# Optimization experiments

Measured on AMD Instinct MI355X. Metric: run time of the kernel, lower is better.

The kernel has to match this reference:

```python
import jax, jax.numpy as jnp
import numpy as np

B, T = 128, 2048
E, OUT, HID = 8, 32, 64          # num_experts, kan_out_features, gru_hidden_dim
GRID_SIZE, ORDER = 5, 3          # standard efficient-kan defaults
KCOEF = GRID_SIZE + ORDER        # B-spline basis functions per input feature


def make_grid():
    # extended knot grid on [-1, 1], length GRID_SIZE + 2*ORDER + 1
    h = 2.0 / GRID_SIZE
    return jnp.arange(-ORDER, GRID_SIZE + ORDER + 1, dtype=jnp.float32) * h - 1.0


def b_splines(x, grid):
    # x: [..., in_features] -> [..., in_features, KCOEF] via Cox-de Boor recursion
    x = x[..., None]
    b = ((x >= grid[:-1]) & (x < grid[1:])).astype(x.dtype)
    for k in range(1, ORDER + 1):
        left = (x - grid[:-(k + 1)]) / (grid[k:-1] - grid[:-(k + 1)])
        right = (grid[k + 1:] - x) / (grid[k + 1:] - grid[1:-k])
        b = left * b[..., :-1] + right * b[..., 1:]
    return b


def kan_moe(x, gate_w, gate_b, base_w, spline_w, grid):
    # x: [B,T,in=1]; dense softmax-gated mixture of KANLinear experts
    gate = jax.nn.softmax(x @ gate_w + gate_b, axis=-1)                 # [B,T,E]
    base_out = jnp.einsum('bti,eoi->bteo', jax.nn.silu(x), base_w)      # [B,T,E,OUT]
    bs = b_splines(x, grid).reshape(x.shape[0], x.shape[1], -1)         # [B,T,in*KCOEF]
    spline_out = jnp.einsum('btk,eok->bteo', bs, spline_w)              # [B,T,E,OUT]
    return jnp.einsum('bte,bteo->bto', gate, base_out + spline_out)     # [B,T,OUT]


def gru(x, w_ih, w_hh, b_ih, b_hh):
    # PyTorch GRU convention: gates ordered (r, z, n); batch_first semantics
    xp = jnp.einsum('btf,gf->btg', x, w_ih) + b_ih                      # [B,T,3H]

    def step(h, xt):
        hp = h @ w_hh.T + b_hh
        xr, xz, xn = jnp.split(xt, 3, axis=-1)
        hr, hz, hn = jnp.split(hp, 3, axis=-1)
        r = jax.nn.sigmoid(xr + hr)
        z = jax.nn.sigmoid(xz + hz)
        n = jnp.tanh(xn + r * hn)
        h = (1.0 - z) * n + z * h
        return h, h

    h0 = jnp.zeros((x.shape[0], HID), x.dtype)
    _, hs = jax.lax.scan(step, h0, jnp.swapaxes(xp, 0, 1))
    return jnp.swapaxes(hs, 0, 1)                                       # [B,T,H]


def setup_inputs() -> dict:
    key = jax.random.key(0)
    ks = jax.random.split(key, 12)
    def n(k, shape, scale=0.1):
        return jax.random.normal(k, shape, jnp.float32) * scale
    return {
        'a': jax.random.normal(ks[0], (B, T, 1), jnp.float32),
        'd': jax.random.normal(ks[1], (B, T, 1), jnp.float32),
        'gate_w_a': n(ks[2], (1, E)), 'gate_b_a': jnp.zeros((E,), jnp.float32),
        'base_w_a': n(ks[3], (E, OUT, 1)), 'spline_w_a': n(ks[4], (E, OUT, KCOEF)),
        'gate_w_d': n(ks[5], (1, E)), 'gate_b_d': jnp.zeros((E,), jnp.float32),
        'base_w_d': n(ks[6], (E, OUT, 1)), 'spline_w_d': n(ks[7], (E, OUT, KCOEF)),
        'conv_w': n(ks[8], (OUT, OUT, 5)), 'conv_b': jnp.zeros((OUT,), jnp.float32),
        'w_ih': n(ks[9], (3 * HID, OUT)), 'w_hh': n(ks[10], (3 * HID, HID)),
        'b_ih': jnp.zeros((3 * HID,), jnp.float32), 'b_hh': jnp.zeros((3 * HID,), jnp.float32),
    }


def reference(a, d, gate_w_a, gate_b_a, base_w_a, spline_w_a,
              gate_w_d, gate_b_d, base_w_d, spline_w_d,
              conv_w, conv_b, w_ih, w_hh, b_ih, b_hh):
    grid = make_grid()
    fa = kan_moe(a, gate_w_a, gate_b_a, base_w_a, spline_w_a, grid)     # trend features
    fd = kan_moe(d, gate_w_d, gate_b_d, base_w_d, spline_w_d, grid)     # residual features
    # TemporalBlock: permute -> Conv1d(padding='same') -> ReLU -> permute back
    xc = jnp.swapaxes(fa, 1, 2)                                         # [B,C,T]
    yc = jax.lax.conv_general_dilated(
        xc, conv_w, (1,), 'SAME', dimension_numbers=('NCH', 'OIH', 'NCH')
    ) + conv_b[None, :, None]
    trend = jnp.swapaxes(jax.nn.relu(yc), 1, 2)                         # [B,T,OUT]
    ctx = gru(fd, w_ih, w_hh, b_ih, b_hh)                               # [B,T,HID]
    # dropout is identity in eval mode
    return jnp.concatenate([trend, ctx], axis=-1)                       # [B,T,OUT+HID]
```

## Files before the change

### kernel.cpp

```cpp
#include <hip/hip_runtime.h>
#include <cstdint>

typedef _Float16 half2_t __attribute__((ext_vector_type(2)));

#define B_   128
#define T_   2048
#define E_   8
#define OUT_ 32
#define HID_ 64
#define KC_  8
#define TILE_A 128
#define NSEG 4
#define SEGT (T_ / NSEG)
#define WUPC 4
#define CH_  32

__device__ __forceinline__ float frcp(float x) { return __builtin_amdgcn_rcpf(x); }
__device__ __forceinline__ float exp2_(float x) {
#if __has_builtin(__builtin_amdgcn_exp2f)
  return __builtin_amdgcn_exp2f(x);
#else
  return exp2f(x);
#endif
}
__device__ __forceinline__ float fsig(float x) { return frcp(1.0f + __expf(-x)); }

__device__ __forceinline__ float fdot2_(half2_t a, half2_t b, float c) {
#if __has_builtin(__builtin_amdgcn_fdot2)
  return __builtin_amdgcn_fdot2(a, b, c, false);
#else
  return fmaf((float)a.x, (float)b.x, fmaf((float)a.y, (float)b.y, c));
#endif
}

__device__ __forceinline__ half2_t u2h2(unsigned u) {
  return __builtin_bit_cast(half2_t, u);
}
__device__ __forceinline__ half2_t packh2(float a, float b) {
  half2_t h; h.x = (_Float16)a; h.y = (_Float16)b; return h;
}

#define NLOG2E  (-1.4426950408889634f)
#define N2LOG2E (-2.8853900817779268f)

__device__ __forceinline__ void kan_scalars(float x, const float* gwr, const float* gbr,
                                            float& silu, float* gate, float* bs) {
  silu = x * fsig(x);
  float le[E_];
  float m = -1e30f;
#pragma unroll
  for (int e = 0; e < E_; ++e) { le[e] = fmaf(x, gwr[e], gbr[e]); m = fmaxf(m, le[e]); }
  float s = 0.f;
#pragma unroll
  for (int e = 0; e < E_; ++e) { gate[e] = __expf(le[e] - m); s += gate[e]; }
  float inv = frcp(s);
#pragma unroll
  for (int e = 0; e < E_; ++e) gate[e] *= inv;
  float g[12];
#pragma unroll
  for (int i = 0; i < 12; ++i) g[i] = (float)(i - 3) * 0.4f - 1.0f;
  float bb[11];
#pragma unroll
  for (int i = 0; i < 11; ++i) bb[i] = (x >= g[i] && x < g[i + 1]) ? 1.0f : 0.0f;
#pragma unroll
  for (int k = 1; k <= 3; ++k) {
#pragma unroll
    for (int i = 0; i < 11 - k; ++i) {
      const float dl = 1.0f / (g[i + k] - g[i]);
      const float dr = 1.0f / (g[i + k + 1] - g[i + 1]);
      float left  = (x - g[i]) * dl;
      float right = (g[i + k + 1] - x) * dr;
      bb[i] = left * bb[i] + right * bb[i + 1];
    }
  }
#pragma unroll
  for (int i = 0; i < KC_; ++i) bs[i] = bb[i];
}

__global__ __launch_bounds__(256, 1) void fused3_kernel(
    const float* __restrict__ a, const float* __restrict__ d,
    const float* __restrict__ gwa, const float* __restrict__ gba,
    const float* __restrict__ bwa, const float* __restrict__ swa,
    const float* __restrict__ gwd, const float* __restrict__ gbd,
    const float* __restrict__ bwd, const float* __restrict__ swd,
    const float* __restrict__ cw, const float* __restrict__ cb,
    const float* __restrict__ wih_g, const float* __restrict__ whh_g,
    const float* __restrict__ bih_g, const float* __restrict__ bhh_g,
    float* __restrict__ out)
{
  __shared__ __align__(16) char smem_[47360];
  const int tid = threadIdx.x;

  if (blockIdx.x < NSEG * B_) {
    auto xqrz   = (unsigned (*)[CH_][64])smem_;
    auto xqn    = (_Float16 (*)[CH_][64])(smem_ + 16384);
    auto packsw = (float (*)[CH_][16])(smem_ + 24576);
    auto hbc    = (unsigned short*)(smem_ + 30720);

    const int b = blockIdx.x & (B_ - 1);
    const int seg = blockIdx.x >> 7;
    const int tstart = (seg == 0) ? 0 : (seg * SEGT - WUPC * CH_);
    const int wup = (seg == 0) ? 0 : WUPC;
    const int nch = ((seg == 0) ? SEGT : (SEGT + WUPC * CH_)) / CH_;
    const int w = tid >> 6;
    const int ln = tid & 63;
    const size_t db = (size_t)b * T_;
    float* outrow = out + db * 96 + 32;
    const uint4* hq4 = (const uint4*)hbc;

    half2_t whhp[3][32];
    float bhh3[3];
    uint4 u0, u1, u2, u3, u4, u5, u6, u7;
    if (w == 0) {
#pragma unroll
      for (int g3 = 0; g3 < 3; ++g3) {
        const float sc = (g3 == 2) ? N2LOG2E : NLOG2E;
        const int g = g3 * 64 + ln;
#pragma unroll
        for (int i = 0; i < 64; i += 4) {
          const float4 v = *(const float4*)&whh_g[(size_t)g * 64 + i];
          whhp[g3][i / 2]     = packh2(v.x * sc, v.y * sc);
          whhp[g3][i / 2 + 1] = packh2(v.z * sc, v.w * sc);
        }
        bhh3[g3] = bhh_g[g] * sc;
      }
      hbc[ln] = __builtin_bit_cast(unsigned short, (_Float16)0.0f);
      asm volatile("" ::: "memory");
      u0 = hq4[0]; u1 = hq4[1]; u2 = hq4[2]; u3 = hq4[3];
      u4 = hq4[4]; u5 = hq4[5]; u6 = hq4[6]; u7 = hq4[7];
    }

    float A_[E_];
    half2_t Beh[E_][4];
    float bihr = 0.f;
    float gwrd[E_], gbrd[E_];
    const int p3 = (w >= 1) ? (w - 1) : 0;
    if (w >= 1) {
      const float sc = (p3 == 2) ? N2LOG2E : NLOG2E;
      const int g = p3 * 64 + ln;
      float wihr[32];
#pragma unroll
      for (int i = 0; i < 32; i += 4) {
        float4 v = *(const float4*)&wih_g[(size_t)g * 32 + i];
        wihr[i] = v.x * sc; wihr[i + 1] = v.y * sc;
        wihr[i + 2] = v.z * sc; wihr[i + 3] = v.w * sc;
      }
      bihr = bih_g[g] * sc;
#pragma unroll
      for (int e = 0; e < E_; ++e) { gwrd[e] = gwd[e]; gbrd[e] = gbd[e]; }
#pragma unroll
      for (int e = 0; e < E_; ++e) {
        float acc = 0.f;
#pragma unroll 4
        for (int c = 0; c < 32; c += 4) {
          const float4 bv = *(const float4*)&bwd[e * OUT_ + c];
          acc = fmaf(wihr[c], bv.x, acc);
          acc = fmaf(wihr[c + 1], bv.y, acc);
          acc = fmaf(wihr[c + 2], bv.z, acc);
          acc = fmaf(wihr[c + 3], bv.w, acc);
        }
        A_[e] = acc;
      }
#pragma unroll
      for (int e = 0; e < E_; ++e) {
        float bk[KC_];
#pragma unroll
        for (int k = 0; k < KC_; ++k) bk[k] = 0.f;
#pragma unroll 4
        for (int c = 0; c < 32; ++c) {
          const float4 s0 = *(const float4*)&swd[(e * OUT_ + c) * KC_ + 0];
          const float4 s1 = *(const float4*)&swd[(e * OUT_ + c) * KC_ + 4];
          const float wc = wihr[c];
          bk[0] = fmaf(wc, s0.x, bk[0]); bk[1] = fmaf(wc, s0.y, bk[1]);
          bk[2] = fmaf(wc, s0.z, bk[2]); bk[3] = fmaf(wc, s0.w, bk[3]);
          bk[4] = fmaf(wc, s1.x, bk[4]); bk[5] = fmaf(wc, s1.y, bk[5]);
          bk[6] = fmaf(wc, s1.z, bk[6]); bk[7] = fmaf(wc, s1.w, bk[7]);
        }
#pragma unroll
        for (int q = 0; q < 4; ++q) Beh[e][q] = packh2(bk[2 * q], bk[2 * q + 1]);
      }
    }

    float h = 0.0f;

    for (int ic = 0; ic <= nch; ++ic) {
      if (w >= 1 && ic < nch) {
        const int p = ic & 1;
        if (ln < CH_) {
          const float x = d[db + tstart + ic * CH_ + ln];
          float silu, gate[E_], bs[KC_];
          kan_scalars(x, gwrd, gbrd, silu, gate, bs);
          float* prow = &packsw[p3][ln][0];
          *(float4*)&prow[0] = *(float4*)&gate[0];
          *(float4*)&prow[4] = *(float4*)&gate[4];
          prow[8] = silu;
          half2_t* bsp = (half2_t*)&prow[10];
#pragma unroll
          for (int q = 0; q < 4; ++q) bsp[q] = packh2(bs[2 * q], bs[2 * q + 1]);
        }
        asm volatile("" ::: "memory");
#pragma unroll 2
        for (int t = 0; t < CH_; ++t) {
          const float* pr = &packsw[p3][t][0];
          const float4 g0 = *(const float4*)&pr[0];
          const float4 g1 = *(const float4*)&pr[4];
          const float silu_t = pr[8];
          const half2_t* bsp = (const half2_t*)&pr[10];
          const half2_t b0 = bsp[0], b1 = bsp[1], b2 = bsp[2], b3 = bsp[3];
          float acc = bihr;
          {
            float in0 = silu_t * A_[0];
            in0 = fdot2_(b0, Beh[0][0], in0); in0 = fdot2_(b1, Beh[0][1], in0);
            in0 = fdot2_(b2, Beh[0][2], in0); in0 = fdot2_(b3, Beh[0][3], in0);
            acc = fmaf(g0.x, in0, acc);
            float in1 = silu_t * A_[1];
            in1 = fdot2_(b0, Beh[1][0], in1); in1 = fdot2_(b1, Beh[1][1], in1);
            in1 = fdot2_(b2, Beh[1][2], in1); in1 = fdot2_(b3, Beh[1][3], in1);
            acc = fmaf(g0.y, in1, acc);
            float in2 = silu_t * A_[2];
            in2 = fdot2_(b0, Beh[2][0], in2); in2 = fdot2_(b1, Beh[2][1], in2);
            in2 = fdot2_(b2, Beh[2][2], in2); in2 = fdot2_(b3, Beh[2][3], in2);
            acc = fmaf(g0.z, in2, acc);
            float in3 = silu_t * A_[3];
            in3 = fdot2_(b0, Beh[3][0], in3); in3 = fdot2_(b1, Beh[3][1], in3);
            in3 = fdot2_(b2, Beh[3][2], in3); in3 = fdot2_(b3, Beh[3][3], in3);
            acc = fmaf(g0.w, in3, acc);
            float in4 = silu_t * A_[4];
            in4 = fdot2_(b0, Beh[4][0], in4); in4 = fdot2_(b1, Beh[4][1], in4);
            in4 = fdot2_(b2, Beh[4][2], in4); in4 = fdot2_(b3, Beh[4][3], in4);
            acc = fmaf(g1.x, in4, acc);
            float in5 = silu_t * A_[5];
            in5 = fdot2_(b0, Beh[5][0], in5); in5 = fdot2_(b1, Beh[5][1], in5);
            in5 = fdot2_(b2, Beh[5][2], in5); in5 = fdot2_(b3, Beh[5][3], in5);
            acc = fmaf(g1.y, in5, acc);
            float in6 = silu_t * A_[6];
            in6 = fdot2_(b0, Beh[6][0], in6); in6 = fdot2_(b1, Beh[6][1], in6);
            in6 = fdot2_(b2, Beh[6][2], in6); in6 = fdot2_(b3, Beh[6][3], in6);
            acc = fmaf(g1.z, in6, acc);
            float in7 = silu_t * A_[7];
            in7 = fdot2_(b0, Beh[7][0], in7); in7 = fdot2_(b1, Beh[7][1], in7);
            in7 = fdot2_(b2, Beh[7][2], in7); in7 = fdot2_(b3, Beh[7][3], in7);
            acc = fmaf(g1.w, in7, acc);
          }
          if (p3 == 0)      ((_Float16*)&xqrz[p][t][ln])[0] = (_Float16)acc;
          else if (p3 == 1) ((_Float16*)&xqrz[p][t][ln])[1] = (_Float16)acc;
          else              xqn[p][t][ln] = (_Float16)acc;
        }
      }

      if (w == 0 && ic >= 1) {
        const int jc = ic - 1;
        const int p = jc & 1;
        const int tb = tstart + jc * CH_;
        const bool do_store = (jc >= wup);
        half2_t rz0 = u2h2(xqrz[p][0][ln]);
        float xr = (float)rz0.x, xz = (float)rz0.y;
        float xn = (float)xqn[p][0][ln];
        __builtin_amdgcn_s_setprio(1);
#pragma unroll 1
        for (int s = 0; s < CH_; ++s) {
          float ar0 = bhh3[0], ar1 = xr, ar2 = 0.f, ar3 = 0.f;
          float az0 = bhh3[1], az1 = xz, az2 = 0.f, az3 = 0.f;
          float an0 = bhh3[2], an1 = 0.f, an2 = 0.f, an3 = 0.f;
          {
            const half2_t q0 = u2h2(u0.x), q1 = u2h2(u0.y), q2 = u2h2(u0.z), q3 = u2h2(u0.w);
            ar0 = fdot2_(whhp[0][0], q0, ar0); ar1 = fdot2_(whhp[0][1], q1, ar1);
            ar2 = fdot2_(whhp[0][2], q2, ar2); ar3 = fdot2_(whhp[0][3], q3, ar3);
            az0 = fdot2_(whhp[1][0], q0, az0); az1 = fdot2_(whhp[1][1], q1, az1);
            az2 = fdot2_(whhp[1][2], q2, az2); az3 = fdot2_(whhp[1][3], q3, az3);
            an0 = fdot2_(whhp[2][0], q0, an0); an1 = fdot2_(whhp[2][1], q1, an1);
            an2 = fdot2_(whhp[2][2], q2, an2); an3 = fdot2_(whhp[2][3], q3, an3);
          }
          {
            const half2_t q0 = u2h2(u1.x), q1 = u2h2(u1.y), q2 = u2h2(u1.z), q3 = u2h2(u1.w);
            ar0 = fdot2_(whhp[0][4], q0, ar0); ar1 = fdot2_(whhp[0][5], q1, ar1);
            ar2 = fdot2_(whhp[0][6], q2, ar2); ar3 = fdot2_(whhp[0][7], q3, ar3);
            az0 = fdot2_(whhp[1][4], q0, az0); az1 = fdot2_(whhp[1][5], q1, az1);
            az2 = fdot2_(whhp[1][6], q2, az2); az3 = fdot2_(whhp[1][7], q3, az3);
            an0 = fdot2_(whhp[2][4], q0, an0); an1 = fdot2_(whhp[2][5], q1, an1);
            an2 = fdot2_(whhp[2][6], q2, an2); an3 = fdot2_(whhp[2][7], q3, an3);
          }
          {
            const half2_t q0 = u2h2(u2.x), q1 = u2h2(u2.y), q2 = u2h2(u2.z), q3 = u2h2(u2.w);
            ar0 = fdot2_(whhp[0][8], q0, ar0); ar1 = fdot2_(whhp[0][9], q1, ar1);
            ar2 = fdot2_(whhp[0][10], q2, ar2); ar3 = fdot2_(whhp[0][11], q3, ar3);
            az0 = fdot2_(whhp[1][8], q0, az0); az1 = fdot2_(whhp[1][9], q1, az1);
            az2 = fdot2_(whhp[1][10], q2, az2); az3 = fdot2_(whhp[1][11], q3, az3);
            an0 = fdot2_(whhp[2][8], q0, an0); an1 = fdot2_(whhp[2][9], q1, an1);
            an2 = fdot2_(whhp[2][10], q2, an2); an3 = fdot2_(whhp[2][11], q3, an3);
          }
          {
            const half2_t q0 = u2h2(u3.x), q1 = u2h2(u3.y), q2 = u2h2(u3.z), q3 = u2h2(u3.w);
            ar0 = fdot2_(whhp[0][12], q0, ar0); ar1 = fdot2_(whhp[0][13], q1, ar1);
            ar2 = fdot2_(whhp[0][14], q2, ar2); ar3 = fdot2_(whhp[0][15], q3, ar3);
            az0 = fdot2_(whhp[1][12], q0, az0); az1 = fdot2_(whhp[1][13], q1, az1);
            az2 = fdot2_(whhp[1][14], q2, az2); az3 = fdot2_(whhp[1][15], q3, az3);
            an0 = fdot2_(whhp[2][12], q0, an0); an1 = fdot2_(whhp[2][13], q1, an1);
            an2 = fdot2_(whhp[2][14], q2, an2); an3 = fdot2_(whhp[2][15], q3, an3);
          }
          {
            const half2_t q0 = u2h2(u4.x), q1 = u2h2(u4.y), q2 = u2h2(u4.z), q3 = u2h2(u4.w);
            ar0 = fdot2_(whhp[0][16], q0, ar0); ar1 = fdot2_(whhp[0][17], q1, ar1);
            ar2 = fdot2_(whhp[0][18], q2, ar2); ar3 = fdot2_(whhp[0][19], q3, ar3);
            az0 = fdot2_(whhp[1][16], q0, az0); az1 = fdot2_(whhp[1][17], q1, az1);
            az2 = fdot2_(whhp[1][18], q2, az2); az3 = fdot2_(whhp[1][19], q3, az3);
            an0 = fdot2_(whhp[2][16], q0, an0); an1 = fdot2_(whhp[2][17], q1, an1);
            an2 = fdot2_(whhp[2][18], q2, an2); an3 = fdot2_(whhp[2][19], q3, an3);
          }
          {
            const half2_t q0 = u2h2(u5.x), q1 = u2h2(u5.y), q2 = u2h2(u5.z), q3 = u2h2(u5.w);
            ar0 = fdot2_(whhp[0][20], q0, ar0); ar1 = fdot2_(whhp[0][21], q1, ar1);
            ar2 = fdot2_(whhp[0][22], q2, ar2); ar3 = fdot2_(whhp[0][23], q3, ar3);
            az0 = fdot2_(whhp[1][20], q0, az0); az1 = fdot2_(whhp[1][21], q1, az1);
            az2 = fdot2_(whhp[1][22], q2, az2); az3 = fdot2_(whhp[1][23], q3, az3);
            an0 = fdot2_(whhp[2][20], q0, an0); an1 = fdot2_(whhp[2][21], q1, an1);
            an2 = fdot2_(whhp[2][22], q2, an2); an3 = fdot2_(whhp[2][23], q3, an3);
          }
          {
            const half2_t q0 = u2h2(u6.x), q1 = u2h2(u6.y), q2 = u2h2(u6.z), q3 = u2h2(u6.w);
            ar0 = fdot2_(whhp[0][24], q0, ar0); ar1 = fdot2_(whhp[0][25], q1, ar1);
            ar2 = fdot2_(whhp[0][26], q2, ar2); ar3 = fdot2_(whhp[0][27], q3, ar3);
            az0 = fdot2_(whhp[1][24], q0, az0); az1 = fdot2_(whhp[1][25], q1, az1);
            az2 = fdot2_(whhp[1][26], q2, az2); az3 = fdot2_(whhp[1][27], q3, az3);
            an0 = fdot2_(whhp[2][24], q0, an0); an1 = fdot2_(whhp[2][25], q1, an1);
            an2 = fdot2_(whhp[2][26], q2, an2); an3 = fdot2_(whhp[2][27], q3, an3);
          }
          {
            const half2_t q0 = u2h2(u7.x), q1 = u2h2(u7.y), q2 = u2h2(u7.z), q3 = u2h2(u7.w);
            ar0 = fdot2_(whhp[0][28], q0, ar0); ar1 = fdot2_(whhp[0][29], q1, ar1);
            ar2 = fdot2_(whhp[0][30], q2, ar2); ar3 = fdot2_(whhp[0][31], q3, ar3);
            az0 = fdot2_(whhp[1][28], q0, az0); az1 = fdot2_(whhp[1][29], q1, az1);
            az2 = fdot2_(whhp[1][30], q2, az2); az3 = fdot2_(whhp[1][31], q3, az3);
            an0 = fdot2_(whhp[2][28], q0, an0); an1 = fdot2_(whhp[2][29], q1, an1);
            an2 = fdot2_(whhp[2][30], q2, an2); an3 = fdot2_(whhp[2][31], q3, an3);
          }
          const float hr = (ar0 + ar1) + (ar2 + ar3);
          const float hz = (az0 + az1) + (az2 + az3);
          const float hn = (an0 + an1) + (an2 + an3);
          const float r = frcp(1.0f + exp2_(hr));
          const float z = frcp(1.0f + exp2_(hz));
          const float tn = frcp(1.0f + exp2_(fmaf(r, hn, xn)));
          const float n = fmaf(2.0f, tn, -1.0f);
          h = n + z * (h - n);
          hbc[ln] = __builtin_bit_cast(unsigned short, (_Float16)h);
          asm volatile("" ::: "memory");
          const int sn = (s + 1) & (CH_ - 1);
          const unsigned rzn = xqrz[p][sn][ln];
          const _Float16 xnn = xqn[p][sn][ln];
          u0 = hq4[0]; u1 = hq4[1]; u2 = hq4[2]; u3 = hq4[3];
          u4 = hq4[4]; u5 = hq4[5]; u6 = hq4[6]; u7 = hq4[7];
          asm volatile("" ::: "memory");
          if (do_store) outrow[(size_t)(tb + s) * 96 + ln] = h;
          const half2_t rzh = u2h2(rzn);
          xr = (float)rzh.x; xz = (float)rzh.y; xn = (float)xnn;
        }
        __builtin_amdgcn_s_setprio(0);
      }
      __syncthreads();
    }
  } else {
    auto fa  = (float (*)[136])smem_;
    auto cwl = (float (*)[161])(smem_ + 17408);
    auto swl = (float (*)[OUT_][KC_])(smem_ + 38016);
    auto bwl = (float (*)[OUT_])(smem_ + 46208);
    float* gwl = (float*)(smem_ + 47232);
    float* gbl = (float*)(smem_ + 47264);

    for (int i = tid; i < OUT_ * OUT_ * 5; i += 256) cwl[i / 160][i % 160] = cw[i];
    for (int i = tid; i < E_ * OUT_ * KC_; i += 256) ((float*)swl)[i] = swa[i];
    for (int i = tid; i < E_ * OUT_; i += 256) ((float*)bwl)[i] = bwa[i];
    if (tid < E_) { gwl[tid] = gwa[tid]; gbl[tid] = gba[tid]; }
    __syncthreads();

    const int cid = blockIdx.x - NSEG * B_;
#pragma unroll 1
    for (int it = 0; it < 16; ++it) {
      const int gt = cid + it * 128;
      const int bb = gt >> 4;
      const int t0 = (gt & 15) * TILE_A;
      if (tid < TILE_A + 4) {
        const int i = tid;
        const int t = t0 + i - 2;
        const bool inr = (t >= 0) && (t < T_);
        const float x = inr ? a[(size_t)bb * T_ + t] : 0.0f;
        float gwr[E_], gbr[E_];
#pragma unroll
        for (int e = 0; e < E_; ++e) { gwr[e] = gwl[e]; gbr[e] = gbl[e]; }
        float silu, gate[E_], bs[KC_];
        kan_scalars(x, gwr, gbr, silu, gate, bs);
#pragma unroll 4
        for (int cc = 0; cc < OUT_; ++cc) {
          float accb = 0.f, accs = 0.f;
#pragma unroll
          for (int e = 0; e < E_; ++e) {
            accb = fmaf(gate[e], bwl[e][cc], accb);
            const float4 s0 = *(const float4*)&swl[e][cc][0];
            const float4 s1 = *(const float4*)&swl[e][cc][4];
            float dot = bs[0]*s0.x + bs[1]*s0.y + bs[2]*s0.z + bs[3]*s0.w
                      + bs[4]*s1.x + bs[5]*s1.y + bs[6]*s1.z + bs[7]*s1.w;
            accs = fmaf(gate[e], dot, accs);
          }
          fa[cc][i] = inr ? fmaf(silu, accb, accs) : 0.0f;
        }
      }
      __syncthreads();
      {
        const int o = tid & 31;
        const int grp = tid >> 5;
        const float bias = cb[o];
        float acc[16];
#pragma unroll
        for (int q = 0; q < 16; ++q) acc[q] = bias;
        for (int c = 0; c < OUT_; ++c) {
          float col[20];
#pragma unroll
          for (int q = 0; q < 5; ++q)
            *(float4*)&col[q * 4] = *(const float4*)&fa[c][grp * 16 + q * 4];
#pragma unroll
          for (int jj = 0; jj < 5; ++jj) {
            const float wv = cwl[o][c * 5 + jj];
#pragma unroll
            for (int q = 0; q < 16; ++q) acc[q] = fmaf(col[q + jj], wv, acc[q]);
          }
        }
#pragma unroll
        for (int q = 0; q < 16; ++q) {
          const int t = t0 + grp * 16 + q;
          out[((size_t)bb * T_ + t) * 96 + o] = fmaxf(acc[q], 0.0f);
        }
      }
      __syncthreads();
    }
  }
}

extern "C" void kernel_launch(void* const* d_in, const int* in_sizes, int n_in,
                              void* d_out, int out_size, void* d_ws, size_t ws_size,
                              hipStream_t stream) {
  (void)in_sizes; (void)n_in; (void)out_size; (void)d_ws; (void)ws_size;
  const float* a        = (const float*)d_in[0];
  const float* d        = (const float*)d_in[1];
  const float* gate_w_a = (const float*)d_in[2];
  const float* gate_b_a = (const float*)d_in[3];
  const float* base_w_a = (const float*)d_in[4];
  const float* spln_w_a = (const float*)d_in[5];
  const float* gate_w_d = (const float*)d_in[6];
  const float* gate_b_d = (const float*)d_in[7];
  const float* base_w_d = (const float*)d_in[8];
  const float* spln_w_d = (const float*)d_in[9];
  const float* conv_w   = (const float*)d_in[10];
  const float* conv_b   = (const float*)d_in[11];
  const float* w_ih     = (const float*)d_in[12];
  const float* w_hh     = (const float*)d_in[13];
  const float* b_ih     = (const float*)d_in[14];
  const float* b_hh     = (const float*)d_in[15];
  float* out = (float*)d_out;

  fused3_kernel<<<NSEG * B_ + B_, 256, 0, stream>>>(
      a, d, gate_w_a, gate_b_a, base_w_a, spln_w_a,
      gate_w_d, gate_b_d, base_w_d, spln_w_d,
      conv_w, conv_b, w_ih, w_hh, b_ih, b_hh, out);
}
```

Measured before the change: 650.9 us.

## Halve GRU time segments and fold conv trend work into each GRU block

```diff
diff --git a/kernel.cpp b/kernel.cpp
--- a/kernel.cpp
+++ b/kernel.cpp
@@ -10,10 +10,11 @@
 #define HID_ 64
 #define KC_  8
 #define TILE_A 128
-#define NSEG 4
-#define SEGT (T_ / NSEG)
-#define WUPC 4
-#define CH_  32
+#define NSEG 2
+#define SPLIT 1088
+#define WUPC 2
+#define CH_  64
+#define NCHB 17
 
 __device__ __forceinline__ float frcp(float x) { return __builtin_amdgcn_rcpf(x); }
 __device__ __forceinline__ float exp2_(float x) {
@@ -77,7 +78,7 @@
   for (int i = 0; i < KC_; ++i) bs[i] = bb[i];
 }
 
-__global__ __launch_bounds__(256, 1) void fused3_kernel(
+__global__ __launch_bounds__(256, 1) void fused5_kernel(
     const float* __restrict__ a, const float* __restrict__ d,
     const float* __restrict__ gwa, const float* __restrict__ gba,
     const float* __restrict__ bwa, const float* __restrict__ swa,
@@ -88,277 +89,277 @@
     const float* __restrict__ bih_g, const float* __restrict__ bhh_g,
     float* __restrict__ out)
 {
-  __shared__ __align__(16) char smem_[47360];
+  __shared__ __align__(16) char smem_[61568];
   const int tid = threadIdx.x;
 
-  if (blockIdx.x < NSEG * B_) {
-    auto xqrz   = (unsigned (*)[CH_][64])smem_;
-    auto xqn    = (_Float16 (*)[CH_][64])(smem_ + 16384);
-    auto packsw = (float (*)[CH_][16])(smem_ + 24576);
-    auto hbc    = (unsigned short*)(smem_ + 30720);
-
-    const int b = blockIdx.x & (B_ - 1);
-    const int seg = blockIdx.x >> 7;
-    const int tstart = (seg == 0) ? 0 : (seg * SEGT - WUPC * CH_);
-    const int wup = (seg == 0) ? 0 : WUPC;
-    const int nch = ((seg == 0) ? SEGT : (SEGT + WUPC * CH_)) / CH_;
-    const int w = tid >> 6;
-    const int ln = tid & 63;
-    const size_t db = (size_t)b * T_;
-    float* outrow = out + db * 96 + 32;
-    const uint4* hq4 = (const uint4*)hbc;
-
-    half2_t whhp[3][32];
-    float bhh3[3];
-    uint4 u0, u1, u2, u3, u4, u5, u6, u7;
-    if (w == 0) {
-#pragma unroll
-      for (int g3 = 0; g3 < 3; ++g3) {
-        const float sc = (g3 == 2) ? N2LOG2E : NLOG2E;
-        const int g = g3 * 64 + ln;
-#pragma unroll
-        for (int i = 0; i < 64; i += 4) {
-          const float4 v = *(const float4*)&whh_g[(size_t)g * 64 + i];
-          whhp[g3][i / 2]     = packh2(v.x * sc, v.y * sc);
-          whhp[g3][i / 2 + 1] = packh2(v.z * sc, v.w * sc);
-        }
-        bhh3[g3] = bhh_g[g] * sc;
-      }
-      hbc[ln] = __builtin_bit_cast(unsigned short, (_Float16)0.0f);
+  auto xqrz   = (unsigned (*)[CH_][64])smem_;
+  auto xqn    = (_Float16 (*)[CH_][64])(smem_ + 32768);
+  auto packsw = (float (*)[CH_][16])(smem_ + 49152);
+  auto hbc    = (unsigned short*)(smem_ + 61440);
+
+  const int bid = (int)blockIdx.x;
+  const int b = bid & (B_ - 1);
+  const int seg = bid >> 7;
+  const int tstart = (seg == 0) ? 0 : (SPLIT - WUPC * CH_);
+  const int wup = (seg == 0) ? 0 : WUPC;
+  const int w = tid >> 6;
+  const int ln = tid & 63;
+  const size_t db = (size_t)b * T_;
+  float* outrow = out + db * 96 + 32;
+  const uint4* hq4 = (const uint4*)hbc;
+
+  half2_t whhp[3][32];
+  float bhh3[3];
+  uint4 u0, u1, u2, u3, u4, u5, u6, u7;
+  if (w == 0) {
+#pragma unroll
+    for (int g3 = 0; g3 < 3; ++g3) {
+      const float sc = (g3 == 2) ? N2LOG2E : NLOG2E;
+      const int g = g3 * 64 + ln;
+#pragma unroll
+      for (int i = 0; i < 64; i += 4) {
+        const float4 v = *(const float4*)&whh_g[(size_t)g * 64 + i];
+        whhp[g3][i / 2]     = packh2(v.x * sc, v.y * sc);
+        whhp[g3][i / 2 + 1] = packh2(v.z * sc, v.w * sc);
+      }
+      bhh3[g3] = bhh_g[g] * sc;
+    }
+    hbc[ln] = __builtin_bit_cast(unsigned short, (_Float16)0.0f);
+    asm volatile("" ::: "memory");
+    u0 = hq4[0]; u1 = hq4[1]; u2 = hq4[2]; u3 = hq4[3];
+    u4 = hq4[4]; u5 = hq4[5]; u6 = hq4[6]; u7 = hq4[7];
+  }
+
+  float A_[E_];
+  half2_t Beh[E_][4];
+  float bihr = 0.f;
+  float gwrd[E_], gbrd[E_];
+  const int p3 = (w >= 1) ? (w - 1) : 0;
+  if (w >= 1) {
+    const float sc = (p3 == 2) ? N2LOG2E : NLOG2E;
+    const int g = p3 * 64 + ln;
+    float wihr[32];
+#pragma unroll
+    for (int i = 0; i < 32; i += 4) {
+      float4 v = *(const float4*)&wih_g[(size_t)g * 32 + i];
+      wihr[i] = v.x * sc; wihr[i + 1] = v.y * sc;
+      wihr[i + 2] = v.z * sc; wihr[i + 3] = v.w * sc;
+    }
+    bihr = bih_g[g] * sc;
+#pragma unroll
+    for (int e = 0; e < E_; ++e) { gwrd[e] = gwd[e]; gbrd[e] = gbd[e]; }
+#pragma unroll
+    for (int e = 0; e < E_; ++e) {
+      float acc = 0.f;
+#pragma unroll 4
+      for (int c = 0; c < 32; c += 4) {
+        const float4 bv = *(const float4*)&bwd[e * OUT_ + c];
+        acc = fmaf(wihr[c], bv.x, acc);
+        acc = fmaf(wihr[c + 1], bv.y, acc);
+        acc = fmaf(wihr[c + 2], bv.z, acc);
+        acc = fmaf(wihr[c + 3], bv.w, acc);
+      }
+      A_[e] = acc;
+    }
+#pragma unroll
+    for (int e = 0; e < E_; ++e) {
+      float bk[KC_];
+#pragma unroll
+      for (int k = 0; k < KC_; ++k) bk[k] = 0.f;
+#pragma unroll 4
+      for (int c = 0; c < 32; ++c) {
+        const float4 s0 = *(const float4*)&swd[(e * OUT_ + c) * KC_ + 0];
+        const float4 s1 = *(const float4*)&swd[(e * OUT_ + c) * KC_ + 4];
+        const float wc = wihr[c];
+        bk[0] = fmaf(wc, s0.x, bk[0]); bk[1] = fmaf(wc, s0.y, bk[1]);
+        bk[2] = fmaf(wc, s0.z, bk[2]); bk[3] = fmaf(wc, s0.w, bk[3]);
+        bk[4] = fmaf(wc, s1.x, bk[4]); bk[5] = fmaf(wc, s1.y, bk[5]);
+        bk[6] = fmaf(wc, s1.z, bk[6]); bk[7] = fmaf(wc, s1.w, bk[7]);
+      }
+#pragma unroll
+      for (int q = 0; q < 4; ++q) Beh[e][q] = packh2(bk[2 * q], bk[2 * q + 1]);
+    }
+  }
+
+  float h = 0.0f;
+
+  for (int ic = 0; ic <= NCHB; ++ic) {
+    if (w >= 1 && ic < NCHB) {
+      const int p = ic & 1;
+      {
+        const float x = d[db + tstart + ic * CH_ + ln];
+        float silu, gate[E_], bs[KC_];
+        kan_scalars(x, gwrd, gbrd, silu, gate, bs);
+        float* prow = &packsw[p3][ln][0];
+        *(float4*)&prow[0] = *(float4*)&gate[0];
+        *(float4*)&prow[4] = *(float4*)&gate[4];
+        prow[8] = silu;
+        half2_t* bsp = (half2_t*)&prow[10];
+#pragma unroll
+        for (int q = 0; q < 4; ++q) bsp[q] = packh2(bs[2 * q], bs[2 * q + 1]);
+      }
       asm volatile("" ::: "memory");
-      u0 = hq4[0]; u1 = hq4[1]; u2 = hq4[2]; u3 = hq4[3];
-      u4 = hq4[4]; u5 = hq4[5]; u6 = hq4[6]; u7 = hq4[7];
-    }
-
-    float A_[E_];
-    half2_t Beh[E_][4];
-    float bihr = 0.f;
-    float gwrd[E_], gbrd[E_];
-    const int p3 = (w >= 1) ? (w - 1) : 0;
-    if (w >= 1) {
-      const float sc = (p3 == 2) ? N2LOG2E : NLOG2E;
-      const int g = p3 * 64 + ln;
-      float wihr[32];
-#pragma unroll
-      for (int i = 0; i < 32; i += 4) {
-        float4 v = *(const float4*)&wih_g[(size_t)g * 32 + i];
-        wihr[i] = v.x * sc; wihr[i + 1] = v.y * sc;
-        wihr[i + 2] = v.z * sc; wihr[i + 3] = v.w * sc;
-      }
-      bihr = bih_g[g] * sc;
-#pragma unroll
-      for (int e = 0; e < E_; ++e) { gwrd[e] = gwd[e]; gbrd[e] = gbd[e]; }
-#pragma unroll
-      for (int e = 0; e < E_; ++e) {
-        float acc = 0.f;
-#pragma unroll 4
-        for (int c = 0; c < 32; c += 4) {
-          const float4 bv = *(const float4*)&bwd[e * OUT_ + c];
-          acc = fmaf(wihr[c], bv.x, acc);
-          acc = fmaf(wihr[c + 1], bv.y, acc);
-          acc = fmaf(wihr[c + 2], bv.z, acc);
-          acc = fmaf(wihr[c + 3], bv.w, acc);
-        }
-        A_[e] = acc;
-      }
-#pragma unroll
-      for (int e = 0; e < E_; ++e) {
-        float bk[KC_];
-#pragma unroll
-        for (int k = 0; k < KC_; ++k) bk[k] = 0.f;
-#pragma unroll 4
-        for (int c = 0; c < 32; ++c) {
-          const float4 s0 = *(const float4*)&swd[(e * OUT_ + c) * KC_ + 0];
-          const float4 s1 = *(const float4*)&swd[(e * OUT_ + c) * KC_ + 4];
-          const float wc = wihr[c];
-          bk[0] = fmaf(wc, s0.x, bk[0]); bk[1] = fmaf(wc, s0.y, bk[1]);
-          bk[2] = fmaf(wc, s0.z, bk[2]); bk[3] = fmaf(wc, s0.w, bk[3]);
-          bk[4] = fmaf(wc, s1.x, bk[4]); bk[5] = fmaf(wc, s1.y, bk[5]);
-          bk[6] = fmaf(wc, s1.z, bk[6]); bk[7] = fmaf(wc, s1.w, bk[7]);
-        }
-#pragma unroll
-        for (int q = 0; q < 4; ++q) Beh[e][q] = packh2(bk[2 * q], bk[2 * q + 1]);
-      }
-    }
-
-    float h = 0.0f;
-
-    for (int ic = 0; ic <= nch; ++ic) {
-      if (w >= 1 && ic < nch) {
-        const int p = ic & 1;
-        if (ln < CH_) {
-          const float x = d[db + tstart + ic * CH_ + ln];
-          float silu, gate[E_], bs[KC_];
-          kan_scalars(x, gwrd, gbrd, silu, gate, bs);
-          float* prow = &packsw[p3][ln][0];
-          *(float4*)&prow[0] = *(float4*)&gate[0];
-          *(float4*)&prow[4] = *(float4*)&gate[4];
-          prow[8] = silu;
-          half2_t* bsp = (half2_t*)&prow[10];
-#pragma unroll
-          for (int q = 0; q < 4; ++q) bsp[q] = packh2(bs[2 * q], bs[2 * q + 1]);
-        }
+#pragma unroll 2
+      for (int t = 0; t < CH_; ++t) {
+        const float* pr = &packsw[p3][t][0];
+        const float4 g0 = *(const float4*)&pr[0];
+        const float4 g1 = *(const float4*)&pr[4];
+        const float silu_t = pr[8];
+        const half2_t* bsp = (const half2_t*)&pr[10];
+        const half2_t b0 = bsp[0], b1 = bsp[1], b2 = bsp[2], b3 = bsp[3];
+        float acc = bihr;
+        {
+          float in0 = silu_t * A_[0];
+          in0 = fdot2_(b0, Beh[0][0], in0); in0 = fdot2_(b1, Beh[0][1], in0);
+          in0 = fdot2_(b2, Beh[0][2], in0); in0 = fdot2_(b3, Beh[0][3], in0);
+          acc = fmaf(g0.x, in0, acc);
+          float in1 = silu_t * A_[1];
+          in1 = fdot2_(b0, Beh[1][0], in1); in1 = fdot2_(b1, Beh[1][1], in1);
+          in1 = fdot2_(b2, Beh[1][2], in1); in1 = fdot2_(b3, Beh[1][3], in1);
+          acc = fmaf(g0.y, in1, acc);
+          float in2 = silu_t * A_[2];
+          in2 = fdot2_(b0, Beh[2][0], in2); in2 = fdot2_(b1, Beh[2][1], in2);
+          in2 = fdot2_(b2, Beh[2][2], in2); in2 = fdot2_(b3, Beh[2][3], in2);
+          acc = fmaf(g0.z, in2, acc);
+          float in3 = silu_t * A_[3];
+          in3 = fdot2_(b0, Beh[3][0], in3); in3 = fdot2_(b1, Beh[3][1], in3);
+          in3 = fdot2_(b2, Beh[3][2], in3); in3 = fdot2_(b3, Beh[3][3], in3);
+          acc = fmaf(g0.w, in3, acc);
+          float in4 = silu_t * A_[4];
+          in4 = fdot2_(b0, Beh[4][0], in4); in4 = fdot2_(b1, Beh[4][1], in4);
+          in4 = fdot2_(b2, Beh[4][2], in4); in4 = fdot2_(b3, Beh[4][3], in4);
+          acc = fmaf(g1.x, in4, acc);
+          float in5 = silu_t * A_[5];
+          in5 = fdot2_(b0, Beh[5][0], in5); in5 = fdot2_(b1, Beh[5][1], in5);
+          in5 = fdot2_(b2, Beh[5][2], in5); in5 = fdot2_(b3, Beh[5][3], in5);
+          acc = fmaf(g1.y, in5, acc);
+          float in6 = silu_t * A_[6];
+          in6 = fdot2_(b0, Beh[6][0], in6); in6 = fdot2_(b1, Beh[6][1], in6);
+          in6 = fdot2_(b2, Beh[6][2], in6); in6 = fdot2_(b3, Beh[6][3], in6);
+          acc = fmaf(g1.z, in6, acc);
+          float in7 = silu_t * A_[7];
+          in7 = fdot2_(b0, Beh[7][0], in7); in7 = fdot2_(b1, Beh[7][1], in7);
+          in7 = fdot2_(b2, Beh[7][2], in7); in7 = fdot2_(b3, Beh[7][3], in7);
+          acc = fmaf(g1.w, in7, acc);
+        }
+        if (p3 == 0)      ((_Float16*)&xqrz[p][t][ln])[0] = (_Float16)acc;
+        else if (p3 == 1) ((_Float16*)&xqrz[p][t][ln])[1] = (_Float16)acc;
+        else              xqn[p][t][ln] = (_Float16)acc;
+      }
+    }
+
+    if (w == 0 && ic >= 1) {
+      const int jc = ic - 1;
+      const int p = jc & 1;
+      const int tb = tstart + jc * CH_;
+      const bool do_store = (jc >= wup);
+      half2_t rz0 = u2h2(xqrz[p][0][ln]);
+      float xr = (float)rz0.x, xz = (float)rz0.y;
+      float xn = (float)xqn[p][0][ln];
+      __builtin_amdgcn_s_setprio(1);
+#pragma unroll 1
+      for (int s = 0; s < CH_; ++s) {
+        float ar0 = bhh3[0], ar1 = xr, ar2 = 0.f, ar3 = 0.f;
+        float az0 = bhh3[1], az1 = xz, az2 = 0.f, az3 = 0.f;
+        float an0 = bhh3[2], an1 = 0.f, an2 = 0.f, an3 = 0.f;
+        {
+          const half2_t q0 = u2h2(u0.x), q1 = u2h2(u0.y), q2 = u2h2(u0.z), q3 = u2h2(u0.w);
+          ar0 = fdot2_(whhp[0][0], q0, ar0); ar1 = fdot2_(whhp[0][1], q1, ar1);
+          ar2 = fdot2_(whhp[0][2], q2, ar2); ar3 = fdot2_(whhp[0][3], q3, ar3);
+          az0 = fdot2_(whhp[1][0], q0, az0); az1 = fdot2_(whhp[1][1], q1, az1);
+          az2 = fdot2_(whhp[1][2], q2, az2); az3 = fdot2_(whhp[1][3], q3, az3);
+          an0 = fdot2_(whhp[2][0], q0, an0); an1 = fdot2_(whhp[2][1], q1, an1);
+          an2 = fdot2_(whhp[2][2], q2, an2); an3 = fdot2_(whhp[2][3], q3, an3);
+        }
+        {
+          const half2_t q0 = u2h2(u1.x), q1 = u2h2(u1.y), q2 = u2h2(u1.z), q3 = u2h2(u1.w);
+          ar0 = fdot2_(whhp[0][4], q0, ar0); ar1 = fdot2_(whhp[0][5], q1, ar1);
+          ar2 = fdot2_(whhp[0][6], q2, ar2); ar3 = fdot2_(whhp[0][7], q3, ar3);
+          az0 = fdot2_(whhp[1][4], q0, az0); az1 = fdot2_(whhp[1][5], q1, az1);
+          az2 = fdot2_(whhp[1][6], q2, az2); az3 = fdot2_(whhp[1][7], q3, az3);
+          an0 = fdot2_(whhp[2][4], q0, an0); an1 = fdot2_(whhp[2][5], q1, an1);
+          an2 = fdot2_(whhp[2][6], q2, an2); an3 = fdot2_(whhp[2][7], q3, an3);
+        }
+        {
+          const half2_t q0 = u2h2(u2.x), q1 = u2h2(u2.y), q2 = u2h2(u2.z), q3 = u2h2(u2.w);
+          ar0 = fdot2_(whhp[0][8], q0, ar0); ar1 = fdot2_(whhp[0][9], q1, ar1);
+          ar2 = fdot2_(whhp[0][10], q2, ar2); ar3 = fdot2_(whhp[0][11], q3, ar3);
+          az0 = fdot2_(whhp[1][8], q0, az0); az1 = fdot2_(whhp[1][9], q1, az1);
+          az2 = fdot2_(whhp[1][10], q2, az2); az3 = fdot2_(whhp[1][11], q3, az3);
+          an0 = fdot2_(whhp[2][8], q0, an0); an1 = fdot2_(whhp[2][9], q1, an1);
+          an2 = fdot2_(whhp[2][10], q2, an2); an3 = fdot2_(whhp[2][11], q3, an3);
+        }
+        {
+          const half2_t q0 = u2h2(u3.x), q1 = u2h2(u3.y), q2 = u2h2(u3.z), q3 = u2h2(u3.w);
+          ar0 = fdot2_(whhp[0][12], q0, ar0); ar1 = fdot2_(whhp[0][13], q1, ar1);
+          ar2 = fdot2_(whhp[0][14], q2, ar2); ar3 = fdot2_(whhp[0][15], q3, ar3);
+          az0 = fdot2_(whhp[1][12], q0, az0); az1 = fdot2_(whhp[1][13], q1, az1);
+          az2 = fdot2_(whhp[1][14], q2, az2); az3 = fdot2_(whhp[1][15], q3, az3);
+          an0 = fdot2_(whhp[2][12], q0, an0); an1 = fdot2_(whhp[2][13], q1, an1);
+          an2 = fdot2_(whhp[2][14], q2, an2); an3 = fdot2_(whhp[2][15], q3, an3);
+        }
+        {
+          const half2_t q0 = u2h2(u4.x), q1 = u2h2(u4.y), q2 = u2h2(u4.z), q3 = u2h2(u4.w);
+          ar0 = fdot2_(whhp[0][16], q0, ar0); ar1 = fdot2_(whhp[0][17], q1, ar1);
+          ar2 = fdot2_(whhp[0][18], q2, ar2); ar3 = fdot2_(whhp[0][19], q3, ar3);
+          az0 = fdot2_(whhp[1][16], q0, az0); az1 = fdot2_(whhp[1][17], q1, az1);
+          az2 = fdot2_(whhp[1][18], q2, az2); az3 = fdot2_(whhp[1][19], q3, az3);
+          an0 = fdot2_(whhp[2][16], q0, an0); an1 = fdot2_(whhp[2][17], q1, an1);
+          an2 = fdot2_(whhp[2][18], q2, an2); an3 = fdot2_(whhp[2][19], q3, an3);
+        }
+        {
+          const half2_t q0 = u2h2(u5.x), q1 = u2h2(u5.y), q2 = u2h2(u5.z), q3 = u2h2(u5.w);
+          ar0 = fdot2_(whhp[0][20], q0, ar0); ar1 = fdot2_(whhp[0][21], q1, ar1);
+          ar2 = fdot2_(whhp[0][22], q2, ar2); ar3 = fdot2_(whhp[0][23], q3, ar3);
+          az0 = fdot2_(whhp[1][20], q0, az0); az1 = fdot2_(whhp[1][21], q1, az1);
+          az2 = fdot2_(whhp[1][22], q2, az2); az3 = fdot2_(whhp[1][23], q3, az3);
+          an0 = fdot2_(whhp[2][20], q0, an0); an1 = fdot2_(whhp[2][21], q1, an1);
+          an2 = fdot2_(whhp[2][22], q2, an2); an3 = fdot2_(whhp[2][23], q3, an3);
+        }
+        {
+          const half2_t q0 = u2h2(u6.x), q1 = u2h2(u6.y), q2 = u2h2(u6.z), q3 = u2h2(u6.w);
+          ar0 = fdot2_(whhp[0][24], q0, ar0); ar1 = fdot2_(whhp[0][25], q1, ar1);
+          ar2 = fdot2_(whhp[0][26], q2, ar2); ar3 = fdot2_(whhp[0][27], q3, ar3);
+          az0 = fdot2_(whhp[1][24], q0, az0); az1 = fdot2_(whhp[1][25], q1, az1);
+          az2 = fdot2_(whhp[1][26], q2, az2); az3 = fdot2_(whhp[1][27], q3, az3);
+          an0 = fdot2_(whhp[2][24], q0, an0); an1 = fdot2_(whhp[2][25], q1, an1);
+          an2 = fdot2_(whhp[2][26], q2, an2); an3 = fdot2_(whhp[2][27], q3, an3);
+        }
+        {
+          const half2_t q0 = u2h2(u7.x), q1 = u2h2(u7.y), q2 = u2h2(u7.z), q3 = u2h2(u7.w);
+          ar0 = fdot2_(whhp[0][28], q0, ar0); ar1 = fdot2_(whhp[0][29], q1, ar1);
+          ar2 = fdot2_(whhp[0][30], q2, ar2); ar3 = fdot2_(whhp[0][31], q3, ar3);
+          az0 = fdot2_(whhp[1][28], q0, az0); az1 = fdot2_(whhp[1][29], q1, az1);
+          az2 = fdot2_(whhp[1][30], q2, az2); az3 = fdot2_(whhp[1][31], q3, az3);
+          an0 = fdot2_(whhp[2][28], q0, an0); an1 = fdot2_(whhp[2][29], q1, an1);
+          an2 = fdot2_(whhp[2][30], q2, an2); an3 = fdot2_(whhp[2][31], q3, an3);
+        }
+        const float hr = (ar0 + ar1) + (ar2 + ar3);
+        const float hz = (az0 + az1) + (az2 + az3);
+        const float hn = (an0 + an1) + (an2 + an3);
+        const float r = frcp(1.0f + exp2_(hr));
+        const float z = frcp(1.0f + exp2_(hz));
+        const float tn = frcp(1.0f + exp2_(fmaf(r, hn, xn)));
+        const float n = fmaf(2.0f, tn, -1.0f);
+        h = n + z * (h - n);
+        hbc[ln] = __builtin_bit_cast(unsigned short, (_Float16)h);
         asm volatile("" ::: "memory");
-#pragma unroll 2
-        for (int t = 0; t < CH_; ++t) {
-          const float* pr = &packsw[p3][t][0];
-          const float4 g0 = *(const float4*)&pr[0];
-          const float4 g1 = *(const float4*)&pr[4];
-          const float silu_t = pr[8];
-          const half2_t* bsp = (const half2_t*)&pr[10];
-          const half2_t b0 = bsp[0], b1 = bsp[1], b2 = bsp[2], b3 = bsp[3];
-          float acc = bihr;
-          {
-            float in0 = silu_t * A_[0];
-            in0 = fdot2_(b0, Beh[0][0], in0); in0 = fdot2_(b1, Beh[0][1], in0);
-            in0 = fdot2_(b2, Beh[0][2], in0); in0 = fdot2_(b3, Beh[0][3], in0);
-            acc = fmaf(g0.x, in0, acc);
-            float in1 = silu_t * A_[1];
-            in1 = fdot2_(b0, Beh[1][0], in1); in1 = fdot2_(b1, Beh[1][1], in1);
-            in1 = fdot2_(b2, Beh[1][2], in1); in1 = fdot2_(b3, Beh[1][3], in1);
-            acc = fmaf(g0.y, in1, acc);
-            float in2 = silu_t * A_[2];
-            in2 = fdot2_(b0, Beh[2][0], in2); in2 = fdot2_(b1, Beh[2][1], in2);
-            in2 = fdot2_(b2, Beh[2][2], in2); in2 = fdot2_(b3, Beh[2][3], in2);
-            acc = fmaf(g0.z, in2, acc);
-            float in3 = silu_t * A_[3];
-            in3 = fdot2_(b0, Beh[3][0], in3); in3 = fdot2_(b1, Beh[3][1], in3);
-            in3 = fdot2_(b2, Beh[3][2], in3); in3 = fdot2_(b3, Beh[3][3], in3);
-            acc = fmaf(g0.w, in3, acc);
-            float in4 = silu_t * A_[4];
-            in4 = fdot2_(b0, Beh[4][0], in4); in4 = fdot2_(b1, Beh[4][1], in4);
-            in4 = fdot2_(b2, Beh[4][2], in4); in4 = fdot2_(b3, Beh[4][3], in4);
-            acc = fmaf(g1.x, in4, acc);
-            float in5 = silu_t * A_[5];
-            in5 = fdot2_(b0, Beh[5][0], in5); in5 = fdot2_(b1, Beh[5][1], in5);
-            in5 = fdot2_(b2, Beh[5][2], in5); in5 = fdot2_(b3, Beh[5][3], in5);
-            acc = fmaf(g1.y, in5, acc);
-            float in6 = silu_t * A_[6];
-            in6 = fdot2_(b0, Beh[6][0], in6); in6 = fdot2_(b1, Beh[6][1], in6);
-            in6 = fdot2_(b2, Beh[6][2], in6); in6 = fdot2_(b3, Beh[6][3], in6);
-            acc = fmaf(g1.z, in6, acc);
-            float in7 = silu_t * A_[7];
-            in7 = fdot2_(b0, Beh[7][0], in7); in7 = fdot2_(b1, Beh[7][1], in7);
-            in7 = fdot2_(b2, Beh[7][2], in7); in7 = fdot2_(b3, Beh[7][3], in7);
-            acc = fmaf(g1.w, in7, acc);
-          }
-          if (p3 == 0)      ((_Float16*)&xqrz[p][t][ln])[0] = (_Float16)acc;
-          else if (p3 == 1) ((_Float16*)&xqrz[p][t][ln])[1] = (_Float16)acc;
-          else              xqn[p][t][ln] = (_Float16)acc;
-        }
-      }
-
-      if (w == 0 && ic >= 1) {
-        const int jc = ic - 1;
-        const int p = jc & 1;
-        const int tb = tstart + jc * CH_;
-        const bool do_store = (jc >= wup);
-        half2_t rz0 = u2h2(xqrz[p][0][ln]);
-        float xr = (float)rz0.x, xz = (float)rz0.y;
-        float xn = (float)xqn[p][0][ln];
-        __builtin_amdgcn_s_setprio(1);
-#pragma unroll 1
-        for (int s = 0; s < CH_; ++s) {
-          float ar0 = bhh3[0], ar1 = xr, ar2 = 0.f, ar3 = 0.f;
-          float az0 = bhh3[1], az1 = xz, az2 = 0.f, az3 = 0.f;
-          float an0 = bhh3[2], an1 = 0.f, an2 = 0.f, an3 = 0.f;
-          {
-            const half2_t q0 = u2h2(u0.x), q1 = u2h2(u0.y), q2 = u2h2(u0.z), q3 = u2h2(u0.w);
-            ar0 = fdot2_(whhp[0][0], q0, ar0); ar1 = fdot2_(whhp[0][1], q1, ar1);
-            ar2 = fdot2_(whhp[0][2], q2, ar2); ar3 = fdot2_(whhp[0][3], q3, ar3);
-            az0 = fdot2_(whhp[1][0], q0, az0); az1 = fdot2_(whhp[1][1], q1, az1);
-            az2 = fdot2_(whhp[1][2], q2, az2); az3 = fdot2_(whhp[1][3], q3, az3);
-            an0 = fdot2_(whhp[2][0], q0, an0); an1 = fdot2_(whhp[2][1], q1, an1);
-            an2 = fdot2_(whhp[2][2], q2, an2); an3 = fdot2_(whhp[2][3], q3, an3);
-          }
-          {
-            const half2_t q0 = u2h2(u1.x), q1 = u2h2(u1.y), q2 = u2h2(u1.z), q3 = u2h2(u1.w);
-            ar0 = fdot2_(whhp[0][4], q0, ar0); ar1 = fdot2_(whhp[0][5], q1, ar1);
-            ar2 = fdot2_(whhp[0][6], q2, ar2); ar3 = fdot2_(whhp[0][7], q3, ar3);
-            az0 = fdot2_(whhp[1][4], q0, az0); az1 = fdot2_(whhp[1][5], q1, az1);
-            az2 = fdot2_(whhp[1][6], q2, az2); az3 = fdot2_(whhp[1][7], q3, az3);
-            an0 = fdot2_(whhp[2][4], q0, an0); an1 = fdot2_(whhp[2][5], q1, an1);
-            an2 = fdot2_(whhp[2][6], q2, an2); an3 = fdot2_(whhp[2][7], q3, an3);
-          }
-          {
-            const half2_t q0 = u2h2(u2.x), q1 = u2h2(u2.y), q2 = u2h2(u2.z), q3 = u2h2(u2.w);
-            ar0 = fdot2_(whhp[0][8], q0, ar0); ar1 = fdot2_(whhp[0][9], q1, ar1);
-            ar2 = fdot2_(whhp[0][10], q2, ar2); ar3 = fdot2_(whhp[0][11], q3, ar3);
-            az0 = fdot2_(whhp[1][8], q0, az0); az1 = fdot2_(whhp[1][9], q1, az1);
-            az2 = fdot2_(whhp[1][10], q2, az2); az3 = fdot2_(whhp[1][11], q3, az3);
-            an0 = fdot2_(whhp[2][8], q0, an0); an1 = fdot2_(whhp[2][9], q1, an1);
-            an2 = fdot2_(whhp[2][10], q2, an2); an3 = fdot2_(whhp[2][11], q3, an3);
-          }
-          {
-            const half2_t q0 = u2h2(u3.x), q1 = u2h2(u3.y), q2 = u2h2(u3.z), q3 = u2h2(u3.w);
-            ar0 = fdot2_(whhp[0][12], q0, ar0); ar1 = fdot2_(whhp[0][13], q1, ar1);
-            ar2 = fdot2_(whhp[0][14], q2, ar2); ar3 = fdot2_(whhp[0][15], q3, ar3);
-            az0 = fdot2_(whhp[1][12], q0, az0); az1 = fdot2_(whhp[1][13], q1, az1);
-            az2 = fdot2_(whhp[1][14], q2, az2); az3 = fdot2_(whhp[1][15], q3, az3);
-            an0 = fdot2_(whhp[2][12], q0, an0); an1 = fdot2_(whhp[2][13], q1, an1);
-            an2 = fdot2_(whhp[2][14], q2, an2); an3 = fdot2_(whhp[2][15], q3, an3);
-          }
-          {
-            const half2_t q0 = u2h2(u4.x), q1 = u2h2(u4.y), q2 = u2h2(u4.z), q3 = u2h2(u4.w);
-            ar0 = fdot2_(whhp[0][16], q0, ar0); ar1 = fdot2_(whhp[0][17], q1, ar1);
-            ar2 = fdot2_(whhp[0][18], q2, ar2); ar3 = fdot2_(whhp[0][19], q3, ar3);
-            az0 = fdot2_(whhp[1][16], q0, az0); az1 = fdot2_(whhp[1][17], q1, az1);
-            az2 = fdot2_(whhp[1][18], q2, az2); az3 = fdot2_(whhp[1][19], q3, az3);
-            an0 = fdot2_(whhp[2][16], q0, an0); an1 = fdot2_(whhp[2][17], q1, an1);
-            an2 = fdot2_(whhp[2][18], q2, an2); an3 = fdot2_(whhp[2][19], q3, an3);
-          }
-          {
-            const half2_t q0 = u2h2(u5.x), q1 = u2h2(u5.y), q2 = u2h2(u5.z), q3 = u2h2(u5.w);
-            ar0 = fdot2_(whhp[0][20], q0, ar0); ar1 = fdot2_(whhp[0][21], q1, ar1);
-            ar2 = fdot2_(whhp[0][22], q2, ar2); ar3 = fdot2_(whhp[0][23], q3, ar3);
-            az0 = fdot2_(whhp[1][20], q0, az0); az1 = fdot2_(whhp[1][21], q1, az1);
-            az2 = fdot2_(whhp[1][22], q2, az2); az3 = fdot2_(whhp[1][23], q3, az3);
-            an0 = fdot2_(whhp[2][20], q0, an0); an1 = fdot2_(whhp[2][21], q1, an1);
-            an2 = fdot2_(whhp[2][22], q2, an2); an3 = fdot2_(whhp[2][23], q3, an3);
-          }
-          {
-            const half2_t q0 = u2h2(u6.x), q1 = u2h2(u6.y), q2 = u2h2(u6.z), q3 = u2h2(u6.w);
-            ar0 = fdot2_(whhp[0][24], q0, ar0); ar1 = fdot2_(whhp[0][25], q1, ar1);
-            ar2 = fdot2_(whhp[0][26], q2, ar2); ar3 = fdot2_(whhp[0][27], q3, ar3);
-            az0 = fdot2_(whhp[1][24], q0, az0); az1 = fdot2_(whhp[1][25], q1, az1);
-            az2 = fdot2_(whhp[1][26], q2, az2); az3 = fdot2_(whhp[1][27], q3, az3);
-            an0 = fdot2_(whhp[2][24], q0, an0); an1 = fdot2_(whhp[2][25], q1, an1);
-            an2 = fdot2_(whhp[2][26], q2, an2); an3 = fdot2_(whhp[2][27], q3, an3);
-          }
-          {
-            const half2_t q0 = u2h2(u7.x), q1 = u2h2(u7.y), q2 = u2h2(u7.z), q3 = u2h2(u7.w);
-            ar0 = fdot2_(whhp[0][28], q0, ar0); ar1 = fdot2_(whhp[0][29], q1, ar1);
-            ar2 = fdot2_(whhp[0][30], q2, ar2); ar3 = fdot2_(whhp[0][31], q3, ar3);
-            az0 = fdot2_(whhp[1][28], q0, az0); az1 = fdot2_(whhp[1][29], q1, az1);
-            az2 = fdot2_(whhp[1][30], q2, az2); az3 = fdot2_(whhp[1][31], q3, az3);
-            an0 = fdot2_(whhp[2][28], q0, an0); an1 = fdot2_(whhp[2][29], q1, an1);
-            an2 = fdot2_(whhp[2][30], q2, an2); an3 = fdot2_(whhp[2][31], q3, an3);
-          }
-          const float hr = (ar0 + ar1) + (ar2 + ar3);
-          const float hz = (az0 + az1) + (az2 + az3);
-          const float hn = (an0 + an1) + (an2 + an3);
-          const float r = frcp(1.0f + exp2_(hr));
-          const float z = frcp(1.0f + exp2_(hz));
-          const float tn = frcp(1.0f + exp2_(fmaf(r, hn, xn)));
-          const float n = fmaf(2.0f, tn, -1.0f);
-          h = n + z * (h - n);
-          hbc[ln] = __builtin_bit_cast(unsigned short, (_Float16)h);
-          asm volatile("" ::: "memory");
-          const int sn = (s + 1) & (CH_ - 1);
-          const unsigned rzn = xqrz[p][sn][ln];
-          const _Float16 xnn = xqn[p][sn][ln];
-          u0 = hq4[0]; u1 = hq4[1]; u2 = hq4[2]; u3 = hq4[3];
-          u4 = hq4[4]; u5 = hq4[5]; u6 = hq4[6]; u7 = hq4[7];
-          asm volatile("" ::: "memory");
-          if (do_store) outrow[(size_t)(tb + s) * 96 + ln] = h;
-          const half2_t rzh = u2h2(rzn);
-          xr = (float)rzh.x; xz = (float)rzh.y; xn = (float)xnn;
-        }
-        __builtin_amdgcn_s_setprio(0);
-      }
-      __syncthreads();
-    }
-  } else {
+        const int sn = (s + 1) & (CH_ - 1);
+        const unsigned rzn = xqrz[p][sn][ln];
+        const _Float16 xnn = xqn[p][sn][ln];
+        u0 = hq4[0]; u1 = hq4[1]; u2 = hq4[2]; u3 = hq4[3];
+        u4 = hq4[4]; u5 = hq4[5]; u6 = hq4[6]; u7 = hq4[7];
+        asm volatile("" ::: "memory");
+        if (do_store) outrow[(size_t)(tb + s) * 96 + ln] = h;
+        const half2_t rzh = u2h2(rzn);
+        xr = (float)rzh.x; xz = (float)rzh.y; xn = (float)xnn;
+      }
+      __builtin_amdgcn_s_setprio(0);
+    }
+    __syncthreads();
+  }
+
+  {
     auto fa  = (float (*)[136])smem_;
     auto cwl = (float (*)[161])(smem_ + 17408);
     auto swl = (float (*)[OUT_][KC_])(smem_ + 38016);
@@ -372,17 +373,14 @@
     if (tid < E_) { gwl[tid] = gwa[tid]; gbl[tid] = gba[tid]; }
     __syncthreads();
 
-    const int cid = blockIdx.x - NSEG * B_;
 #pragma unroll 1
-    for (int it = 0; it < 16; ++it) {
-      const int gt = cid + it * 128;
-      const int bb = gt >> 4;
-      const int t0 = (gt & 15) * TILE_A;
+    for (int it = 0; it < 8; ++it) {
+      const int t0 = (seg * 8 + it) * TILE_A;
       if (tid < TILE_A + 4) {
         const int i = tid;
         const int t = t0 + i - 2;
         const bool inr = (t >= 0) && (t < T_);
-        const float x = inr ? a[(size_t)bb * T_ + t] : 0.0f;
+        const float x = inr ? a[db + t] : 0.0f;
         float gwr[E_], gbr[E_];
 #pragma unroll
         for (int e = 0; e < E_; ++e) { gwr[e] = gwl[e]; gbr[e] = gbl[e]; }
@@ -426,7 +424,7 @@
 #pragma unroll
         for (int q = 0; q < 16; ++q) {
           const int t = t0 + grp * 16 + q;
-          out[((size_t)bb * T_ + t) * 96 + o] = fmaxf(acc[q], 0.0f);
+          out[(db + t) * 96 + o] = fmaxf(acc[q], 0.0f);
         }
       }
       __syncthreads();
@@ -456,7 +454,7 @@
   const float* b_hh     = (const float*)d_in[15];
   float* out = (float*)d_out;
 
-  fused3_kernel<<<NSEG * B_ + B_, 256, 0, stream>>>(
+  fused5_kernel<<<NSEG * B_, 256, 0, stream>>>(
       a, d, gate_w_a, gate_b_a, base_w_a, spln_w_a,
       gate_w_d, gate_b_d, base_w_d, spln_w_d,
       conv_w, conv_b, w_ih, w_hh, b_ih, b_hh, out);
```

Measured after the change: 580.6 us. 10.8% less time.
